# Performance work log

Hardware: AMD Instinct MI355X
Metric: run time of the kernel (lower is better)

The kernel has to match this reference:

```python
import jax, jax.numpy as jnp
import numpy as np

B, IN, H = 4096, 2048, 2048


def setup_inputs() -> dict:
    key = jax.random.key(0)
    ks = jax.random.split(key, 7)
    s_in = 1.0 / np.sqrt(IN)
    s_h = 1.0 / np.sqrt(H)
    return {
        "x": jax.random.normal(ks[0], (B, IN), jnp.float32),
        "hx": jax.random.normal(ks[1], (B, H), jnp.float32),
        "cx": jax.random.normal(ks[2], (B, H), jnp.float32),
        "Wx": jax.random.normal(ks[3], (4 * H, IN), jnp.float32) * s_in,
        "bx": jax.random.normal(ks[4], (4 * H,), jnp.float32) * s_in,
        "Wh": jax.random.normal(ks[5], (4 * H, H), jnp.float32) * s_h,
        "bh": jax.random.normal(ks[6], (4 * H,), jnp.float32) * s_h,
    }


def reference(x, hx, cx, Wx, bx, Wh, bh):
    # gates: [B, 4H] = x @ Wx^T + bx + hx @ Wh^T + bh
    gates = jnp.einsum('bi,gi->bg', x, Wx) + bx + jnp.einsum('bh,gh->bg', hx, Wh) + bh
    i, f, g, o = jnp.split(gates, 4, axis=1)
    i = jax.nn.sigmoid(i)
    f = jax.nn.sigmoid(f)
    g = jnp.tanh(g)
    o = jax.nn.sigmoid(o)
    cy = f * cx + i * g
    hy = o * jnp.tanh(cy)
    return (hy, cy)
```

## Files before the change

### kernel.cpp

```cpp
#include <hip/hip_runtime.h>
#include <hip/hip_bf16.h>


typedef _Float16 half8 __attribute__((ext_vector_type(8)));
typedef _Float16 half4 __attribute__((ext_vector_type(4)));
typedef float    f32x4 __attribute__((ext_vector_type(4)));

#define H_DIM  2048
#define BH_TOT 8388608
#define NT     128
#define W2_OFF 67108864u

__device__ __forceinline__ void gload_lds16(const void* g, void* l) {
    __builtin_amdgcn_global_load_lds(
        (const __attribute__((address_space(1))) unsigned int*)g,
        (__attribute__((address_space(3))) unsigned int*)l,
        16, 0, 0);
}

__device__ __forceinline__ void barrier_all() {
    __builtin_amdgcn_sched_barrier(0);
    __builtin_amdgcn_s_barrier();
    __builtin_amdgcn_sched_barrier(0);
}

__device__ __forceinline__ float fast_sigmoid(float x) {
    return 1.0f / (1.0f + __expf(-x));
}
__device__ __forceinline__ float fast_tanh(float x) {
    float e = __expf(2.0f * x);
    return 1.0f - 2.0f / (e + 1.0f);
}

__global__ void split_kernel(const float* __restrict__ src,
                             _Float16* __restrict__ dst, int colOff, int n4) {
    const int stride = gridDim.x * blockDim.x;
    for (int i = blockIdx.x * blockDim.x + threadIdx.x; i < n4; i += stride) {
        float4 v = ((const float4*)src)[i];
        int idx = i << 2;
        int r = idx >> 11;
        int c = idx & 2047;
        int k = colOff + c;
        long d = (long)r * 8192 + (k >> 5) * 64 + (k & 31);
        half4 h4, l4;
        float vv[4] = {v.x, v.y, v.z, v.w};
        #pragma unroll
        for (int j = 0; j < 4; ++j) {
            _Float16 h = (_Float16)vv[j];
            h4[j] = h;
            l4[j] = (_Float16)(vv[j] - (float)h);
        }
        *(half4*)&dst[d] = h4;
        *(half4*)&dst[d + 32] = l4;
    }
}

#define MFMA3(AM, WN, ACC)                                                   \
    ACC = __builtin_amdgcn_mfma_f32_16x16x32_f16(AM[0], WN[0], ACC, 0, 0, 0); \
    ACC = __builtin_amdgcn_mfma_f32_16x16x32_f16(AM[0], WN[1], ACC, 0, 0, 0); \
    ACC = __builtin_amdgcn_mfma_f32_16x16x32_f16(AM[1], WN[0], ACC, 0, 0, 0);

__global__ __launch_bounds__(512, 2)
void lstm8p(const char* __restrict__ wsbase,
            const float* __restrict__ bx, const float* __restrict__ bh,
            const float* __restrict__ cx, float* __restrict__ out) {
    __shared__ _Float16 sm[2][2][256 * 64];

    const int t = threadIdx.x;
    const int wid = t >> 6;
    const int l = t & 63;
    const int wr = wid >> 2;
    const int wc = wid & 3;

    const int bid = blockIdx.x;
    const int swz = (bid & 7) * 64 + (bid >> 3);
    const int cb = swz & 31;
    const int rb = swz >> 5;

    const int lr = l >> 3;
    const int ks = ((l & 7) ^ lr) * 8;
    unsigned offA[4], offW[4];
    #pragma unroll
    for (int g = 0; g < 4; ++g) {
        const int rowA = rb * 256 + g * 64 + wid * 8 + lr;
        offA[g] = (unsigned)rowA * 16384u + (unsigned)ks * 2u;
        const int e = g * 64 + wid * 8 + lr;
        const int gc = ((e >> 4) & 3) * H_DIM + cb * 64 + (e >> 6) * 16 + (e & 15);
        offW[g] = W2_OFF + (unsigned)gc * 16384u + (unsigned)ks * 2u;
    }
    const int ldsrow = wid * 8;

    auto STAGE = [&](int kt, int db) {
        const unsigned kb = (unsigned)kt * 128u;
        #pragma unroll
        for (int g = 0; g < 4; ++g)
            gload_lds16(wsbase + offA[g] + kb, (_Float16*)&sm[db][0][(g * 64 + ldsrow) * 64]);
        #pragma unroll
        for (int g = 0; g < 4; ++g)
            gload_lds16(wsbase + offW[g] + kb, (_Float16*)&sm[db][1][(g * 64 + ldsrow) * 64]);
    };

    int laneF[2];
    #pragma unroll
    for (int tm = 0; tm < 2; ++tm)
        laneF[tm] = (l & 15) * 128 + (((tm * 4 + (l >> 4)) ^ (l & 7)) << 4);

    auto LDA = [&](int db, int m, int tm) -> half8 {
        const char* p = (const char*)&sm[db][0][0] + (wr * 128 + m * 16) * 128 + laneF[tm];
        return *(const half8*)p;
    };
    auto LDW = [&](int db, int n, int tm) -> half8 {
        const char* p = (const char*)&sm[db][1][0] + (wc * 64 + n * 16) * 128 + laneF[tm];
        return *(const half8*)p;
    };

    f32x4 acc[8][4];
    #pragma unroll
    for (int m = 0; m < 8; ++m)
        #pragma unroll
        for (int n = 0; n < 4; ++n) acc[m][n] = (f32x4){0.f, 0.f, 0.f, 0.f};

    STAGE(0, 0);
    STAGE(1, 1);
    asm volatile("s_waitcnt vmcnt(8)" ::: "memory");
    barrier_all();

    half8 a[4][2], w[4][2];
    for (int kt = 0; kt < NT; ++kt) {
        const int cur = kt & 1;
        #pragma unroll
        for (int m = 0; m < 4; ++m) { a[m][0] = LDA(cur, m, 0); a[m][1] = LDA(cur, m, 1); }
        #pragma unroll
        for (int n = 0; n < 2; ++n) { w[n][0] = LDW(cur, n, 0); w[n][1] = LDW(cur, n, 1); }
        barrier_all();
        __builtin_amdgcn_s_setprio(1);
        #pragma unroll
        for (int m = 0; m < 4; ++m) {
            MFMA3(a[m], w[0], acc[m][0]);
            MFMA3(a[m], w[1], acc[m][1]);
        }
        __builtin_amdgcn_s_setprio(0);
        barrier_all();
        #pragma unroll
        for (int n = 2; n < 4; ++n) { w[n][0] = LDW(cur, n, 0); w[n][1] = LDW(cur, n, 1); }
        barrier_all();
        __builtin_amdgcn_s_setprio(1);
        #pragma unroll
        for (int m = 0; m < 4; ++m) {
            MFMA3(a[m], w[2], acc[m][2]);
            MFMA3(a[m], w[3], acc[m][3]);
        }
        __builtin_amdgcn_s_setprio(0);
        barrier_all();
        #pragma unroll
        for (int m = 0; m < 4; ++m) { a[m][0] = LDA(cur, m + 4, 0); a[m][1] = LDA(cur, m + 4, 1); }
        barrier_all();
        __builtin_amdgcn_s_setprio(1);
        #pragma unroll
        for (int m = 0; m < 4; ++m) {
            MFMA3(a[m], w[0], acc[m + 4][0]);
            MFMA3(a[m], w[1], acc[m + 4][1]);
        }
        __builtin_amdgcn_s_setprio(0);
        barrier_all();
        if (kt + 2 < NT) STAGE(kt + 2, cur);
        barrier_all();
        __builtin_amdgcn_s_setprio(1);
        #pragma unroll
        for (int m = 0; m < 4; ++m) {
            MFMA3(a[m], w[2], acc[m + 4][2]);
            MFMA3(a[m], w[3], acc[m + 4][3]);
        }
        __builtin_amdgcn_s_setprio(0);
        if (kt < NT - 2) {
            asm volatile("s_waitcnt vmcnt(8)" ::: "memory");
        } else if (kt == NT - 2) {
            asm volatile("s_waitcnt vmcnt(0)" ::: "memory");
        }
        barrier_all();
    }

    const int hcol = cb * 64 + wc * 16 + (l & 15);
    float bs[4];
    #pragma unroll
    for (int g = 0; g < 4; ++g) bs[g] = bx[g * H_DIM + hcol] + bh[g * H_DIM + hcol];
    const int row0 = rb * 256 + wr * 128 + (l >> 4) * 4;
    #pragma unroll
    for (int m = 0; m < 8; ++m) {
        #pragma unroll
        for (int r = 0; r < 4; ++r) {
            const long base = (long)(row0 + m * 16 + r) * H_DIM + hcol;
            const float iv = fast_sigmoid(acc[m][0][r] + bs[0]);
            const float fv = fast_sigmoid(acc[m][1][r] + bs[1]);
            const float gv = fast_tanh(acc[m][2][r] + bs[2]);
            const float ov = fast_sigmoid(acc[m][3][r] + bs[3]);
            const float c0 = cx[base];
            const float cyv = fv * c0 + iv * gv;
            const float hyv = ov * fast_tanh(cyv);
            out[base] = hyv;
            out[BH_TOT + base] = cyv;
        }
    }
}

extern "C" void kernel_launch(void* const* d_in, const int* in_sizes, int n_in,
                              void* d_out, int out_size, void* d_ws, size_t ws_size,
                              hipStream_t stream) {
    (void)in_sizes; (void)n_in; (void)out_size; (void)ws_size;
    const float* x  = (const float*)d_in[0];
    const float* hx = (const float*)d_in[1];
    const float* cx = (const float*)d_in[2];
    const float* Wx = (const float*)d_in[3];
    const float* bx = (const float*)d_in[4];
    const float* Wh = (const float*)d_in[5];
    const float* bh = (const float*)d_in[6];
    float* out = (float*)d_out;

    _Float16* A2 = (_Float16*)d_ws;
    _Float16* W2 = (_Float16*)((char*)d_ws + W2_OFF);

    split_kernel<<<2048, 256, 0, stream>>>(x,  A2, 0,    2097152);
    split_kernel<<<2048, 256, 0, stream>>>(hx, A2, 2048, 2097152);
    split_kernel<<<2048, 256, 0, stream>>>(Wx, W2, 0,    4194304);
    split_kernel<<<2048, 256, 0, stream>>>(Wh, W2, 2048, 4194304);

    lstm8p<<<512, 512, 0, stream>>>((const char*)d_ws, bx, bh, cx, out);
}
```

Before: 921.4 us.

## Fuse split launches, stagger A/W prefetch, unroll K loop, remap block tiles

Merges the four fp16 hi/lo split launches into a single kernel to cut launch overhead. In the GEMM loop it issues the W and A prefetches at different phases, and unrolls the K loop by two so the LDS buffer index is a compile-time constant. It also drops the trailing barrier on the final iteration and the sched_barrier fences around s_barrier, and changes the block-to-tile mapping for L2 locality. Removing the scheduling fences lets the compiler move LDS reads relative to barriers, which risks hazards or a worse instruction schedule.

```diff
diff --git a/kernel.cpp b/kernel.cpp
--- a/kernel.cpp
+++ b/kernel.cpp
@@ -18,12 +18,6 @@
         16, 0, 0);
 }
 
-__device__ __forceinline__ void barrier_all() {
-    __builtin_amdgcn_sched_barrier(0);
-    __builtin_amdgcn_s_barrier();
-    __builtin_amdgcn_sched_barrier(0);
-}
-
 __device__ __forceinline__ float fast_sigmoid(float x) {
     return 1.0f / (1.0f + __expf(-x));
 }
@@ -32,15 +26,26 @@
     return 1.0f - 2.0f / (e + 1.0f);
 }
 
-__global__ void split_kernel(const float* __restrict__ src,
-                             _Float16* __restrict__ dst, int colOff, int n4) {
+__global__ void split_all(const float* __restrict__ x, const float* __restrict__ hx,
+                          const float* __restrict__ Wx, const float* __restrict__ Wh,
+                          _Float16* __restrict__ A2, _Float16* __restrict__ W2) {
     const int stride = gridDim.x * blockDim.x;
-    for (int i = blockIdx.x * blockDim.x + threadIdx.x; i < n4; i += stride) {
-        float4 v = ((const float4*)src)[i];
-        int idx = i << 2;
+    for (int i = blockIdx.x * blockDim.x + threadIdx.x; i < 12582912; i += stride) {
+        const float* src; _Float16* dst; int ri, colOff;
+        if (i < 4194304) {
+            dst = A2;
+            if (i < 2097152) { src = x;  ri = i;           colOff = 0; }
+            else             { src = hx; ri = i - 2097152; colOff = 2048; }
+        } else {
+            dst = W2;
+            int j = i - 4194304;
+            if (j < 4194304) { src = Wx; ri = j;           colOff = 0; }
+            else             { src = Wh; ri = j - 4194304; colOff = 2048; }
+        }
+        float4 v = ((const float4*)src)[ri];
+        int idx = ri << 2;
         int r = idx >> 11;
-        int c = idx & 2047;
-        int k = colOff + c;
+        int k = colOff + (idx & 2047);
         long d = (long)r * 8192 + (k >> 5) * 64 + (k & 31);
         half4 h4, l4;
         float vv[4] = {v.x, v.y, v.z, v.w};
@@ -55,7 +60,7 @@
     }
 }
 
-#define MFMA3(AM, WN, ACC)                                                   \
+#define MFMA3(AM, WN, ACC)                                                    \
     ACC = __builtin_amdgcn_mfma_f32_16x16x32_f16(AM[0], WN[0], ACC, 0, 0, 0); \
     ACC = __builtin_amdgcn_mfma_f32_16x16x32_f16(AM[0], WN[1], ACC, 0, 0, 0); \
     ACC = __builtin_amdgcn_mfma_f32_16x16x32_f16(AM[1], WN[0], ACC, 0, 0, 0);
@@ -73,9 +78,9 @@
     const int wc = wid & 3;
 
     const int bid = blockIdx.x;
-    const int swz = (bid & 7) * 64 + (bid >> 3);
-    const int cb = swz & 31;
-    const int rb = swz >> 5;
+    const int c8 = bid >> 3;
+    const int rb = c8 & 15;
+    const int cb = (bid & 7) * 4 + (c8 >> 4);
 
     const int lr = l >> 3;
     const int ks = ((l & 7) ^ lr) * 8;
@@ -90,11 +95,14 @@
     }
     const int ldsrow = wid * 8;
 
-    auto STAGE = [&](int kt, int db) {
+    auto STAGE_A = [&](int kt, int db) {
         const unsigned kb = (unsigned)kt * 128u;
         #pragma unroll
         for (int g = 0; g < 4; ++g)
             gload_lds16(wsbase + offA[g] + kb, (_Float16*)&sm[db][0][(g * 64 + ldsrow) * 64]);
+    };
+    auto STAGE_W = [&](int kt, int db) {
+        const unsigned kb = (unsigned)kt * 128u;
         #pragma unroll
         for (int g = 0; g < 4; ++g)
             gload_lds16(wsbase + offW[g] + kb, (_Float16*)&sm[db][1][(g * 64 + ldsrow) * 64]);
@@ -120,64 +128,57 @@
         #pragma unroll
         for (int n = 0; n < 4; ++n) acc[m][n] = (f32x4){0.f, 0.f, 0.f, 0.f};
 
-    STAGE(0, 0);
-    STAGE(1, 1);
+    STAGE_W(0, 0); STAGE_A(0, 0);
+    STAGE_W(1, 1); STAGE_A(1, 1);
     asm volatile("s_waitcnt vmcnt(8)" ::: "memory");
-    barrier_all();
-
-    half8 a[4][2], w[4][2];
-    for (int kt = 0; kt < NT; ++kt) {
-        const int cur = kt & 1;
-        #pragma unroll
-        for (int m = 0; m < 4; ++m) { a[m][0] = LDA(cur, m, 0); a[m][1] = LDA(cur, m, 1); }
-        #pragma unroll
-        for (int n = 0; n < 2; ++n) { w[n][0] = LDW(cur, n, 0); w[n][1] = LDW(cur, n, 1); }
-        barrier_all();
-        __builtin_amdgcn_s_setprio(1);
-        #pragma unroll
-        for (int m = 0; m < 4; ++m) {
-            MFMA3(a[m], w[0], acc[m][0]);
-            MFMA3(a[m], w[1], acc[m][1]);
-        }
-        __builtin_amdgcn_s_setprio(0);
-        barrier_all();
-        #pragma unroll
-        for (int n = 2; n < 4; ++n) { w[n][0] = LDW(cur, n, 0); w[n][1] = LDW(cur, n, 1); }
-        barrier_all();
-        __builtin_amdgcn_s_setprio(1);
-        #pragma unroll
-        for (int m = 0; m < 4; ++m) {
-            MFMA3(a[m], w[2], acc[m][2]);
-            MFMA3(a[m], w[3], acc[m][3]);
-        }
-        __builtin_amdgcn_s_setprio(0);
-        barrier_all();
-        #pragma unroll
-        for (int m = 0; m < 4; ++m) { a[m][0] = LDA(cur, m + 4, 0); a[m][1] = LDA(cur, m + 4, 1); }
-        barrier_all();
-        __builtin_amdgcn_s_setprio(1);
-        #pragma unroll
-        for (int m = 0; m < 4; ++m) {
-            MFMA3(a[m], w[0], acc[m + 4][0]);
-            MFMA3(a[m], w[1], acc[m + 4][1]);
-        }
-        __builtin_amdgcn_s_setprio(0);
-        barrier_all();
-        if (kt + 2 < NT) STAGE(kt + 2, cur);
-        barrier_all();
-        __builtin_amdgcn_s_setprio(1);
-        #pragma unroll
-        for (int m = 0; m < 4; ++m) {
-            MFMA3(a[m], w[2], acc[m + 4][2]);
-            MFMA3(a[m], w[3], acc[m + 4][3]);
-        }
+    __builtin_amdgcn_s_barrier();
+
+    auto TILE = [&](const int db, const int kt) {
+        half8 a[4][2], w[4][2];
+        #pragma unroll
+        for (int m = 0; m < 4; ++m) { a[m][0] = LDA(db, m, 0); a[m][1] = LDA(db, m, 1); }
+        #pragma unroll
+        for (int n = 0; n < 2; ++n) { w[n][0] = LDW(db, n, 0); w[n][1] = LDW(db, n, 1); }
+        __builtin_amdgcn_s_barrier();
+        __builtin_amdgcn_s_setprio(1);
+        #pragma unroll
+        for (int m = 0; m < 4; ++m) { MFMA3(a[m], w[0], acc[m][0]); MFMA3(a[m], w[1], acc[m][1]); }
+        __builtin_amdgcn_s_setprio(0);
+        __builtin_amdgcn_s_barrier();
+        #pragma unroll
+        for (int n = 2; n < 4; ++n) { w[n][0] = LDW(db, n, 0); w[n][1] = LDW(db, n, 1); }
+        __builtin_amdgcn_s_barrier();
+        __builtin_amdgcn_s_setprio(1);
+        #pragma unroll
+        for (int m = 0; m < 4; ++m) { MFMA3(a[m], w[2], acc[m][2]); MFMA3(a[m], w[3], acc[m][3]); }
+        __builtin_amdgcn_s_setprio(0);
+        __builtin_amdgcn_s_barrier();
+        #pragma unroll
+        for (int m = 0; m < 4; ++m) { a[m][0] = LDA(db, m + 4, 0); a[m][1] = LDA(db, m + 4, 1); }
+        if (kt + 2 < NT) STAGE_W(kt + 2, db);
+        __builtin_amdgcn_s_barrier();
+        __builtin_amdgcn_s_setprio(1);
+        #pragma unroll
+        for (int m = 0; m < 4; ++m) { MFMA3(a[m], w[0], acc[m + 4][0]); MFMA3(a[m], w[1], acc[m + 4][1]); }
+        __builtin_amdgcn_s_setprio(0);
+        __builtin_amdgcn_s_barrier();
+        if (kt + 2 < NT) STAGE_A(kt + 2, db);
+        __builtin_amdgcn_s_setprio(1);
+        #pragma unroll
+        for (int m = 0; m < 4; ++m) { MFMA3(a[m], w[2], acc[m + 4][2]); MFMA3(a[m], w[3], acc[m + 4][3]); }
         __builtin_amdgcn_s_setprio(0);
         if (kt < NT - 2) {
             asm volatile("s_waitcnt vmcnt(8)" ::: "memory");
+            __builtin_amdgcn_s_barrier();
         } else if (kt == NT - 2) {
             asm volatile("s_waitcnt vmcnt(0)" ::: "memory");
-        }
-        barrier_all();
+            __builtin_amdgcn_s_barrier();
+        }
+    };
+
+    for (int kt = 0; kt < NT; kt += 2) {
+        TILE(0, kt);
+        TILE(1, kt + 1);
     }
 
     const int hcol = cb * 64 + wc * 16 + (l & 15);
@@ -219,10 +220,6 @@
     _Float16* A2 = (_Float16*)d_ws;
     _Float16* W2 = (_Float16*)((char*)d_ws + W2_OFF);
 
-    split_kernel<<<2048, 256, 0, stream>>>(x,  A2, 0,    2097152);
-    split_kernel<<<2048, 256, 0, stream>>>(hx, A2, 2048, 2097152);
-    split_kernel<<<2048, 256, 0, stream>>>(Wx, W2, 0,    4194304);
-    split_kernel<<<2048, 256, 0, stream>>>(Wh, W2, 2048, 4194304);
-
+    split_all<<<2048, 256, 0, stream>>>(x, hx, Wx, Wh, A2, W2);
     lstm8p<<<512, 512, 0, stream>>>((const char*)d_ws, bx, bh, cx, out);
 }
```

After: 828.8 us. -10.0%, faster.
